# Optimization experiments

Measured on AMD Instinct MI355X. Metric: run time of the kernel, lower is better.

Reference implementation:

```python
import jax, jax.numpy as jnp
import numpy as np

N = 20000      # nodes
E = 640000     # edges
HID = 128      # hidden_dim
HEADS = 8
HD = HID // HEADS  # head_dim = 16


def setup_inputs() -> dict:
    key = jax.random.key(0)
    ks = jax.random.split(key, 32)
    s = 1.0 / np.sqrt(HID)
    d = {}
    d["h"] = jax.random.normal(ks[0], (N, HID), jnp.float32)
    d["x"] = jax.random.normal(ks[1], (N, 3), jnp.float32)
    d["src"] = jax.random.randint(ks[2], (E,), 0, N)
    d["dst"] = jax.random.randint(ks[3], (E,), 0, N)
    d["distances"] = jax.random.uniform(ks[4], (E,), jnp.float32)
    d["bpp_edge_bias"] = jax.random.uniform(ks[5], (E,), jnp.float32)
    d["msa_edge_bias"] = jax.random.uniform(ks[6], (E,), jnp.float32)
    d["chem_edge_bias"] = jax.random.uniform(ks[7], (E,), jnp.float32)
    d["relative_offset"] = jax.random.normal(ks[8], (E,), jnp.float32)
    d["chain_break_mask"] = jax.random.uniform(ks[9], (E,), jnp.float32)
    # attention projections (nn.Linear(hidden, hidden): y = x @ W + b)
    for i, nm in enumerate(["Wq", "Wk", "Wv", "Wo"]):
        d[nm] = jax.random.normal(ks[10 + i], (HID, HID), jnp.float32) * s
    for nm in ["bq", "bk", "bv", "bo"]:
        d[nm] = jnp.zeros((HID,), jnp.float32)
    # six Linear(1, heads) edge-bias heads -> weight vector [HEADS] + bias [HEADS]
    for i, nm in enumerate(["dist", "bpp", "msa", "chem", "rel", "chain"]):
        d["w_" + nm] = jax.random.normal(ks[14 + i], (HEADS,), jnp.float32) * 0.1
        d["b_" + nm] = jnp.zeros((HEADS,), jnp.float32)
    # coord_gate: Linear(HID,HID) -> SiLU -> Linear(HID,1) -> Tanh
    d["Wg1"] = jax.random.normal(ks[20], (HID, HID), jnp.float32) * s
    d["bg1"] = jnp.zeros((HID,), jnp.float32)
    d["wg2"] = jax.random.normal(ks[21], (HID, 1), jnp.float32) * s
    d["bg2"] = jnp.zeros((1,), jnp.float32)
    return d


def _edge_bias(feat, w, b):
    # Linear(1, heads) applied to per-edge scalar: [E] -> [E, HEADS]
    return feat[:, None] * w[None, :] + b[None, :]


def reference(h, x, src, dst, distances, bpp_edge_bias, msa_edge_bias,
              chem_edge_bias, relative_offset, chain_break_mask,
              Wq, bq, Wk, bk, Wv, bv, Wo, bo,
              w_dist, b_dist, w_bpp, b_bpp, w_msa, b_msa,
              w_chem, b_chem, w_rel, b_rel, w_chain, b_chain,
              Wg1, bg1, wg2, bg2):
    n = h.shape[0]
    q = (h @ Wq + bq).reshape(n, HEADS, HD)
    k = (h @ Wk + bk).reshape(n, HEADS, HD)
    v = (h @ Wv + bv).reshape(n, HEADS, HD)
    q_src = q[src]   # [E, H, D]
    k_dst = k[dst]
    v_dst = v[dst]
    logits = jnp.einsum('ehd,ehd->eh', q_src, k_dst) / np.sqrt(float(HD))
    logits = (logits
              - _edge_bias(distances * distances, w_dist, b_dist)
              + _edge_bias(bpp_edge_bias, w_bpp, b_bpp)
              + _edge_bias(msa_edge_bias, w_msa, b_msa)
              + _edge_bias(chem_edge_bias, w_chem, b_chem)
              + _edge_bias(relative_offset, w_rel, b_rel)
              + _edge_bias(chain_break_mask, w_chain, b_chain))
    # segment softmax over edges grouped by src node, per head
    m = jax.ops.segment_max(logits, src, num_segments=n)        # [N, H]
    ex = jnp.exp(logits - m[src])                               # [E, H]
    denom = jax.ops.segment_sum(ex, src, num_segments=n)        # [N, H]
    weights = ex / jnp.maximum(denom[src], 1e-9)                # [E, H]
    # weighted scatter-aggregate of values to src nodes
    h_update = jax.ops.segment_sum(v_dst * weights[:, :, None], src,
                                   num_segments=n).reshape(n, HID)
    h_out = h + h_update @ Wo + bo
    # coordinate update
    weights_mean = weights.mean(axis=1)                         # [E]
    disp = jax.ops.segment_sum((x[dst] - x[src]) * weights_mean[:, None],
                               src, num_segments=n)             # [N, 3]
    gate = jnp.tanh(jax.nn.silu(h_out @ Wg1 + bg1) @ wg2 + bg2)  # [N, 1]
    x_out = x + gate * disp
    return h_out, x_out
```

## Files before the change

kernel.cpp:

```cpp
#include <hip/hip_runtime.h>
#include <hip/hip_bf16.h>

#define N_NODES 20000
#define N_EDGES 640000
#define HID 128
#define HEADS 8
#define HD 16
#define NB_SCAN ((N_NODES + 255) / 256)
#define CH 160
#define QKV_BLOCKS 625
#define PREP_BLOCKS 5

typedef __attribute__((ext_vector_type(8))) short bf16x8;
typedef __attribute__((ext_vector_type(4))) float f32x4;

__device__ __forceinline__ float bflo(unsigned u) {
    union { unsigned i; float f; } x; x.i = u << 16; return x.f;
}
__device__ __forceinline__ float bfhi(unsigned u) {
    union { unsigned i; float f; } x; x.i = u & 0xffff0000u; return x.f;
}
__device__ __forceinline__ float bfu(ushort u) {
    union { unsigned i; float f; } x; x.i = ((unsigned)u) << 16; return x.f;
}
__device__ __forceinline__ ushort f2bu(float f) {
    __hip_bfloat16 b = __float2bfloat16(f);
    union { __hip_bfloat16 b; ushort u; } c; c.b = b; return c.u;
}

__global__ __launch_bounds__(256) void hist_prep_kernel(const int* __restrict__ src,
        int* __restrict__ cnt, int* __restrict__ rank,
        const float* __restrict__ Wq, const float* __restrict__ Wk,
        const float* __restrict__ Wv, const float* __restrict__ Wo,
        const float* __restrict__ Wg1, ushort* __restrict__ Wt) {
    if (blockIdx.x < PREP_BLOCKS) {
        const float* srcs[5] = {Wq, Wk, Wv, Wo, Wg1};
        const float* W = srcs[blockIdx.x];
        ushort* out = Wt + (size_t)blockIdx.x * 16384;
        for (int i = threadIdx.x; i < 16384; i += 256) {
            int k = i >> 7, n = i & 127;
            out[n * 128 + k] = f2bu(W[i]);
        }
    } else {
        const int e = (blockIdx.x - PREP_BLOCKS) * 256 + threadIdx.x;
        rank[e] = atomicAdd(&cnt[src[e]], 1);
    }
}

__global__ __launch_bounds__(256) void scan1_kernel(const int* __restrict__ cnt,
        int* __restrict__ startp, int* __restrict__ blockSums, int n) {
    __shared__ int sd[256];
    const int tid = threadIdx.x;
    const int i = blockIdx.x * 256 + tid;
    int xv = (i < n) ? cnt[i] : 0;
    sd[tid] = xv;
    __syncthreads();
#pragma unroll
    for (int off = 1; off < 256; off <<= 1) {
        int tv = (tid >= off) ? sd[tid - off] : 0;
        __syncthreads();
        sd[tid] += tv;
        __syncthreads();
    }
    if (i < n) startp[i] = sd[tid] - xv;
    if (tid == 255) blockSums[blockIdx.x] = sd[255];
}

__global__ __launch_bounds__(128) void scan2_kernel(int* __restrict__ blockSums, int nb) {
    __shared__ int sd[128];
    const int tid = threadIdx.x;
    int xv = (tid < nb) ? blockSums[tid] : 0;
    sd[tid] = xv;
    __syncthreads();
#pragma unroll
    for (int off = 1; off < 128; off <<= 1) {
        int tv = (tid >= off) ? sd[tid - off] : 0;
        __syncthreads();
        sd[tid] += tv;
        __syncthreads();
    }
    if (tid < nb) blockSums[tid] = sd[tid] - xv;
    if (tid == 127) blockSums[nb] = sd[127];
}

__global__ __launch_bounds__(256) void scatter_qkv_kernel(
        const float* __restrict__ h, const ushort* __restrict__ Wt,
        const float* __restrict__ bq, const float* __restrict__ bk,
        const float* __restrict__ bv,
        ushort* __restrict__ qb, ushort* __restrict__ kb, ushort* __restrict__ vb,
        const int* __restrict__ src, const int* __restrict__ dst,
        const float* __restrict__ dist, const float* __restrict__ bpp,
        const float* __restrict__ msa, const float* __restrict__ chem,
        const float* __restrict__ rel, const float* __restrict__ chain,
        const float* __restrict__ w_dist, const float* __restrict__ b_dist,
        const float* __restrict__ w_bpp, const float* __restrict__ b_bpp,
        const float* __restrict__ w_msa, const float* __restrict__ b_msa,
        const float* __restrict__ w_chem, const float* __restrict__ b_chem,
        const float* __restrict__ w_rel, const float* __restrict__ b_rel,
        const float* __restrict__ w_chain, const float* __restrict__ b_chain,
        const int* __restrict__ startp, const int* __restrict__ blockSums,
        const int* __restrict__ rank, const float* __restrict__ x,
        uint4* __restrict__ recs) {
    __shared__ __align__(16) ushort hs[32 * 136];
    const int t = threadIdx.x;
    if (blockIdx.x < QKV_BLOCKS) {
        const int row0 = blockIdx.x * 32;
        for (int i = t; i < 4096; i += 256)
            hs[(i >> 7) * 136 + (i & 127)] = f2bu(h[(size_t)row0 * 128 + i]);
        __syncthreads();
        const int w = t >> 6, lane = t & 63;
        const int rt = w >> 1, half = w & 1;
        const int lrow = lane & 15, lkb = (lane >> 4) * 8;
        bf16x8 a[4];
#pragma unroll
        for (int ks = 0; ks < 4; ++ks)
            a[ks] = *reinterpret_cast<const bf16x8*>(&hs[(rt * 16 + lrow) * 136 + ks * 32 + lkb]);
        const int rbase = row0 + rt * 16 + (lane >> 4) * 4;
#define DO_MAT(MI, BIAS, OUT) \
        for (int ctp = 0; ctp < 4; ++ctp) { \
            const int col = (ctp * 2 + half) * 16 + lrow; \
            f32x4 acc = {0.f, 0.f, 0.f, 0.f}; \
            _Pragma("unroll") \
            for (int ks = 0; ks < 4; ++ks) { \
                bf16x8 b = *reinterpret_cast<const bf16x8*>( \
                    &Wt[MI * 16384 + col * 128 + ks * 32 + lkb]); \
                acc = __builtin_amdgcn_mfma_f32_16x16x32_bf16(a[ks], b, acc, 0, 0, 0); \
            } \
            const float bias = BIAS[col]; \
            _Pragma("unroll") \
            for (int r = 0; r < 4; ++r) \
                OUT[(size_t)(rbase + r) * 128 + col] = f2bu(acc[r] + bias); \
        }
        DO_MAT(0, bq, qb)
        DO_MAT(1, bk, kb)
        DO_MAT(2, bv, vb)
#undef DO_MAT
    } else {
        const int e = (blockIdx.x - QKV_BLOCKS) * 256 + t;
        const int s = src[e];
        const int pos = startp[s] + blockSums[s >> 8] + rank[e];
        const int dn = dst[e];
        const float d2 = dist[e] * dist[e];
        const float f_bpp = bpp[e], f_msa = msa[e], f_chem = chem[e];
        const float f_rel = rel[e], f_chain = chain[e];
        ushort o16[8];
#pragma unroll
        for (int hq = 0; hq < 8; ++hq) {
            float b = -(d2 * w_dist[hq] + b_dist[hq])
                    + (f_bpp * w_bpp[hq] + b_bpp[hq])
                    + (f_msa * w_msa[hq] + b_msa[hq])
                    + (f_chem * w_chem[hq] + b_chem[hq])
                    + (f_rel * w_rel[hq] + b_rel[hq])
                    + (f_chain * w_chain[hq] + b_chain[hq]);
            o16[hq] = f2bu(b);
        }
        uint4 rec0;
        rec0.x = (unsigned)o16[0] | ((unsigned)o16[1] << 16);
        rec0.y = (unsigned)o16[2] | ((unsigned)o16[3] << 16);
        rec0.z = (unsigned)o16[4] | ((unsigned)o16[5] << 16);
        rec0.w = (unsigned)o16[6] | ((unsigned)o16[7] << 16);
        const float* xp = &x[(size_t)dn * 3];
        uint4 rec1;
        rec1.x = (unsigned)dn;
        rec1.y = __float_as_uint(xp[0]);
        rec1.z = __float_as_uint(xp[1]);
        rec1.w = __float_as_uint(xp[2]);
        recs[(size_t)pos * 2]     = rec0;
        recs[(size_t)pos * 2 + 1] = rec1;
    }
}

__global__ __launch_bounds__(256) void node_kernel(const ushort* __restrict__ qb,
        const ushort* __restrict__ kb, const ushort* __restrict__ vb,
        const uint4* __restrict__ recs, const float* __restrict__ x,
        const int* __restrict__ startp, const int* __restrict__ blockSums,
        ushort* __restrict__ hub, float* __restrict__ disp) {
    __shared__ float qLds[4 * 128];
    __shared__ float xsLds[12];
    __shared__ int   sLds[5];
    __shared__ int   dnLds[CH];
    __shared__ float xLds[CH * 3];
    __shared__ __align__(16) ushort biasLds[CH * 8];
    __shared__ float peLds[CH * 8];
    __shared__ float redN[4][32][9];

    const int t = threadIdx.x;
    const int n0 = blockIdx.x * 4;

    for (int i = t; i < 4 * 128; i += 256) qLds[i] = bfu(qb[(size_t)n0 * 128 + i]);
    if (t < 12) xsLds[t] = x[(size_t)n0 * 3 + t];
    if (t < 5) {
        int idx = n0 + t;
        sLds[t] = (idx < N_NODES) ? (startp[idx] + blockSums[idx >> 8]) : N_EDGES;
    }
    __syncthreads();

    const int S0 = sLds[0], S4 = sLds[4];
    const int s1r = sLds[1], s2r = sLds[2], s3r = sLds[3];

    const int eg = t >> 5;
    const int dq = t & 31;
    const int hh = dq >> 2;
    const int jj = dq & 3;
    const int j3 = (jj < 3) ? jj : 0;

    float acc0[4] = {0,0,0,0}, acc1[4] = {0,0,0,0};
    float acc2[4] = {0,0,0,0}, acc3[4] = {0,0,0,0};
    float den0 = 0, den1 = 0, den2 = 0, den3 = 0;
    float adx0 = 0, adx1 = 0, adx2 = 0, adx3 = 0;

    for (int base = S0; base < S4; base += CH) {
        const int en = min(CH, S4 - base);
        __syncthreads();
        if (t < en) {
            const uint4 r0 = recs[(size_t)(base + t) * 2];
            const uint4 r1 = recs[(size_t)(base + t) * 2 + 1];
            *reinterpret_cast<uint4*>(&biasLds[t * 8]) = r0;
            dnLds[t] = (int)r1.x;
            xLds[t * 3 + 0] = __uint_as_float(r1.y);
            xLds[t * 3 + 1] = __uint_as_float(r1.z);
            xLds[t * 3 + 2] = __uint_as_float(r1.w);
        }
        __syncthreads();
        const int np = en * 8;
        for (int p = t; p < np; p += 256) {
            const int e = p >> 3, ha = p & 7;
            const int ge = base + e;
            const int m = (ge >= s1r) + (ge >= s2r) + (ge >= s3r);
            const ushort* krow = kb + (size_t)dnLds[e] * 128 + ha * 16;
            const uint4 ka = *reinterpret_cast<const uint4*>(krow);
            const uint4 kb4 = *reinterpret_cast<const uint4*>(krow + 8);
            const float* qrow = &qLds[m * 128 + ha * 16];
            const unsigned* kau = reinterpret_cast<const unsigned*>(&ka);
            const unsigned* kbu = reinterpret_cast<const unsigned*>(&kb4);
            float s = 0.f;
#pragma unroll
            for (int i = 0; i < 4; ++i) {
                s += bflo(kau[i]) * qrow[2 * i]     + bfhi(kau[i]) * qrow[2 * i + 1];
                s += bflo(kbu[i]) * qrow[8 + 2 * i] + bfhi(kbu[i]) * qrow[8 + 2 * i + 1];
            }
            peLds[p] = __expf(fmaf(s, 0.25f, bfu(biasLds[p])));
        }
        __syncthreads();
#define NODE_C(M, ACC, DEN, ADX) { \
            const int lo = max(sLds[M] - base, 0); \
            const int hi = min(sLds[M + 1] - base, en); \
            const float xsv = xsLds[M * 3 + j3]; \
            for (int e = lo + eg; e < hi; e += 8) { \
                const float pe = peLds[e * 8 + hh]; \
                const ushort4 vv = *reinterpret_cast<const ushort4*>( \
                    vb + (size_t)dnLds[e] * 128 + dq * 4); \
                ACC[0] = fmaf(pe, bfu(vv.x), ACC[0]); \
                ACC[1] = fmaf(pe, bfu(vv.y), ACC[1]); \
                ACC[2] = fmaf(pe, bfu(vv.z), ACC[2]); \
                ACC[3] = fmaf(pe, bfu(vv.w), ACC[3]); \
                DEN += pe; \
                ADX = fmaf(pe, xLds[e * 3 + j3] - xsv, ADX); \
            } }
        NODE_C(0, acc0, den0, adx0)
        NODE_C(1, acc1, den1, adx1)
        NODE_C(2, acc2, den2, adx2)
        NODE_C(3, acc3, den3, adx3)
#undef NODE_C
    }

    const int wv = t >> 6, lane = t & 63;
#define RED_M(M, ACC, DEN, ADX) { \
        float r0 = ACC[0], r1 = ACC[1], r2 = ACC[2], r3 = ACC[3]; \
        float rd = DEN, rx = (jj < 3) ? ADX : 0.f; \
        r0 += __shfl_xor(r0, 32); r1 += __shfl_xor(r1, 32); \
        r2 += __shfl_xor(r2, 32); r3 += __shfl_xor(r3, 32); \
        rd += __shfl_xor(rd, 32); rx += __shfl_xor(rx, 32); \
        if (lane < 32) { \
            redN[wv][lane][0] = r0; redN[wv][lane][1] = r1; \
            redN[wv][lane][2] = r2; redN[wv][lane][3] = r3; \
            redN[wv][lane][4] = rd; redN[wv][lane][5] = rx; \
        } \
        __syncthreads(); \
        if (t < 128) { \
            const int dqr = t >> 2, vi = t & 3; \
            float s = redN[0][dqr][vi] + redN[1][dqr][vi] \
                    + redN[2][dqr][vi] + redN[3][dqr][vi]; \
            float d = redN[0][dqr][4] + redN[1][dqr][4] \
                    + redN[2][dqr][4] + redN[3][dqr][4]; \
            hub[(size_t)(n0 + M) * 128 + t] = f2bu(s / fmaxf(d, 1e-9f)); \
        } \
        if (t < 32) { \
            float v = redN[0][t][5] + redN[1][t][5] + redN[2][t][5] + redN[3][t][5]; \
            float d = redN[0][t][4] + redN[1][t][4] + redN[2][t][4] + redN[3][t][4]; \
            float s = v / fmaxf(d, 1e-9f); \
            s += __shfl_xor(s, 4); s += __shfl_xor(s, 8); s += __shfl_xor(s, 16); \
            if (t < 3) disp[(size_t)(n0 + M) * 3 + t] = s * 0.125f; \
        } \
        __syncthreads(); }
    RED_M(0, acc0, den0, adx0)
    RED_M(1, acc1, den1, adx1)
    RED_M(2, acc2, den2, adx2)
    RED_M(3, acc3, den3, adx3)
#undef RED_M
}

__global__ __launch_bounds__(256) void out_kernel(const float* __restrict__ h,
        const float* __restrict__ x, const ushort* __restrict__ hub,
        const ushort* __restrict__ Wt,
        const float* __restrict__ bo, const float* __restrict__ bg1,
        const float* __restrict__ wg2, const float* __restrict__ bg2,
        const float* __restrict__ disp,
        float* __restrict__ hout, float* __restrict__ xout) {
    __shared__ __align__(16) ushort hus[32 * 136];
    __shared__ __align__(16) ushort hob[32 * 136];
    __shared__ float g1s[32 * 132];
    const int t = threadIdx.x;
    const int row0 = blockIdx.x * 32;
    for (int i = t; i < 4096; i += 256)
        hus[(i >> 7) * 136 + (i & 127)] = hub[(size_t)row0 * 128 + i];
    __syncthreads();
    const int w = t >> 6, lane = t & 63;
    const int rt = w >> 1, half = w & 1;
    const int lrow = lane & 15, lkb = (lane >> 4) * 8;
    const int rloc = rt * 16 + (lane >> 4) * 4;
    bf16x8 a[4];
#pragma unroll
    for (int ks = 0; ks < 4; ++ks)
        a[ks] = *reinterpret_cast<const bf16x8*>(&hus[(rt * 16 + lrow) * 136 + ks * 32 + lkb]);
    for (int ctp = 0; ctp < 4; ++ctp) {
        const int col = (ctp * 2 + half) * 16 + lrow;
        f32x4 acc = {0.f, 0.f, 0.f, 0.f};
#pragma unroll
        for (int ks = 0; ks < 4; ++ks) {
            bf16x8 b = *reinterpret_cast<const bf16x8*>(&Wt[3 * 16384 + col * 128 + ks * 32 + lkb]);
            acc = __builtin_amdgcn_mfma_f32_16x16x32_bf16(a[ks], b, acc, 0, 0, 0);
        }
        const float bias = bo[col];
#pragma unroll
        for (int r = 0; r < 4; ++r) {
            const int row = rloc + r;
            float hv = h[(size_t)(row0 + row) * 128 + col] + acc[r] + bias;
            hout[(size_t)(row0 + row) * 128 + col] = hv;
            hob[row * 136 + col] = f2bu(hv);
        }
    }
    __syncthreads();
#pragma unroll
    for (int ks = 0; ks < 4; ++ks)
        a[ks] = *reinterpret_cast<const bf16x8*>(&hob[(rt * 16 + lrow) * 136 + ks * 32 + lkb]);
    for (int ctp = 0; ctp < 4; ++ctp) {
        const int col = (ctp * 2 + half) * 16 + lrow;
        f32x4 acc = {0.f, 0.f, 0.f, 0.f};
#pragma unroll
        for (int ks = 0; ks < 4; ++ks) {
            bf16x8 b = *reinterpret_cast<const bf16x8*>(&Wt[4 * 16384 + col * 128 + ks * 32 + lkb]);
            acc = __builtin_amdgcn_mfma_f32_16x16x32_bf16(a[ks], b, acc, 0, 0, 0);
        }
        const float bias = bg1[col];
#pragma unroll
        for (int r = 0; r < 4; ++r) {
            float av = acc[r] + bias;
            g1s[(rloc + r) * 132 + col] = av / (1.f + __expf(-av));
        }
    }
    __syncthreads();
    {
        const int r = t >> 3, j = t & 7;
        float partial = 0.f;
        for (int cc = j; cc < 128; cc += 8) partial += g1s[r * 132 + cc] * wg2[cc];
        partial += __shfl_xor(partial, 1);
        partial += __shfl_xor(partial, 2);
        partial += __shfl_xor(partial, 4);
        const float gate = tanhf(partial + bg2[0]);
        if (j < 3) {
            const int row = row0 + r;
            xout[(size_t)row * 3 + j] = x[(size_t)row * 3 + j] + gate * disp[(size_t)row * 3 + j];
        }
    }
}


extern "C" void kernel_launch(void* const* d_in, const int* in_sizes, int n_in,
                              void* d_out, int out_size, void* d_ws, size_t ws_size,
                              hipStream_t stream) {
    const float* h     = (const float*)d_in[0];
    const float* x     = (const float*)d_in[1];
    const int*   src   = (const int*)d_in[2];
    const int*   dst   = (const int*)d_in[3];
    const float* dist  = (const float*)d_in[4];
    const float* bpp   = (const float*)d_in[5];
    const float* msa   = (const float*)d_in[6];
    const float* chem  = (const float*)d_in[7];
    const float* rel   = (const float*)d_in[8];
    const float* chain = (const float*)d_in[9];
    const float* Wq = (const float*)d_in[10];
    const float* Wk = (const float*)d_in[11];
    const float* Wv = (const float*)d_in[12];
    const float* Wo = (const float*)d_in[13];
    const float* bq = (const float*)d_in[14];
    const float* bk = (const float*)d_in[15];
    const float* bv = (const float*)d_in[16];
    const float* bo = (const float*)d_in[17];
    const float* w_dist = (const float*)d_in[18];  const float* b_dist = (const float*)d_in[19];
    const float* w_bpp  = (const float*)d_in[20];  const float* b_bpp  = (const float*)d_in[21];
    const float* w_msa  = (const float*)d_in[22];  const float* b_msa  = (const float*)d_in[23];
    const float* w_chem = (const float*)d_in[24];  const float* b_chem = (const float*)d_in[25];
    const float* w_rel  = (const float*)d_in[26];  const float* b_rel  = (const float*)d_in[27];
    const float* w_chain= (const float*)d_in[28];  const float* b_chain= (const float*)d_in[29];
    const float* Wg1 = (const float*)d_in[30];
    const float* bg1 = (const float*)d_in[31];
    const float* wg2 = (const float*)d_in[32];
    const float* bg2 = (const float*)d_in[33];

    char* wp = (char*)d_ws;
    const size_t NH2 = (size_t)N_NODES * HID * sizeof(ushort);
    ushort* hub   = (ushort*)wp;               wp += NH2;
    ushort* qb    = (ushort*)wp;               wp += NH2;
    ushort* kb    = (ushort*)wp;               wp += NH2;
    ushort* vb    = (ushort*)wp;               wp += NH2;
    uint4*  recs  = (uint4*)wp;                wp += (size_t)N_EDGES * 32;
    float*  disp  = (float*)wp;                wp += (size_t)N_NODES * 3 * sizeof(float);
    int* rank     = (int*)wp;                  wp += (size_t)N_EDGES * sizeof(int);
    int* startp   = (int*)wp;                  wp += (size_t)N_NODES * sizeof(int);
    int* cnt      = (int*)wp;                  wp += (size_t)N_NODES * sizeof(int);
    int* blockSums= (int*)wp;                  wp += (size_t)(NB_SCAN + 1) * sizeof(int);
    ushort* Wt    = (ushort*)wp;               wp += (size_t)5 * 16384 * sizeof(ushort);

    float* hout = (float*)d_out;
    float* xout = hout + (size_t)N_NODES * HID;

    hipMemsetAsync(cnt, 0, (size_t)N_NODES * sizeof(int), stream);
    hipLaunchKernelGGL(hist_prep_kernel, dim3(N_EDGES / 256 + PREP_BLOCKS), dim3(256), 0, stream,
                       src, cnt, rank, Wq, Wk, Wv, Wo, Wg1, Wt);
    hipLaunchKernelGGL(scan1_kernel, dim3(NB_SCAN), dim3(256), 0, stream,
                       cnt, startp, blockSums, N_NODES);
    hipLaunchKernelGGL(scan2_kernel, dim3(1), dim3(128), 0, stream, blockSums, NB_SCAN);
    hipLaunchKernelGGL(scatter_qkv_kernel, dim3(QKV_BLOCKS + N_EDGES / 256), dim3(256), 0, stream,
                       h, Wt, bq, bk, bv, qb, kb, vb,
                       src, dst, dist, bpp, msa, chem, rel, chain,
                       w_dist, b_dist, w_bpp, b_bpp, w_msa, b_msa,
                       w_chem, b_chem, w_rel, b_rel, w_chain, b_chain,
                       startp, blockSums, rank, x, recs);
    hipLaunchKernelGGL(node_kernel, dim3(N_NODES / 4), dim3(256), 0, stream,
                       qb, kb, vb, recs, x, startp, blockSums, hub, disp);
    hipLaunchKernelGGL(out_kernel, dim3(N_NODES / 32), dim3(256), 0, stream,
                       h, x, hub, Wt, bo, bg1, wg2, bg2, disp, hout, xout);
}
```

Baseline: 163.8 us.

## Stage QKV and out-projection tiles in LDS for coalesced vector I/O, unroll edge loops

The QKV projection now writes each bf16 output tile to shared memory and then copies it to global memory with coalesced 16-byte stores, in place of scattered 2-byte stores. The node kernel loads q with vector loads, splits the dot product across four independent accumulators, and unrolls the attention and aggregation edge loops by two to expose more memory-level parallelism. The output kernel stages h into LDS with float4 loads and writes hout with float4 stores, rebuilding the bf16 gate input from the fp32 tile. This adds extra barriers and LDS traffic, and the larger LDS footprint in the output kernel may lower occupancy.

```diff
diff --git a/kernel.cpp b/kernel.cpp
--- a/kernel.cpp
+++ b/kernel.cpp
@@ -115,8 +115,10 @@
 #pragma unroll
         for (int ks = 0; ks < 4; ++ks)
             a[ks] = *reinterpret_cast<const bf16x8*>(&hs[(rt * 16 + lrow) * 136 + ks * 32 + lkb]);
-        const int rbase = row0 + rt * 16 + (lane >> 4) * 4;
+        __syncthreads();
+        const int rloc0 = rt * 16 + (lane >> 4) * 4;
 #define DO_MAT(MI, BIAS, OUT) \
+        { \
         for (int ctp = 0; ctp < 4; ++ctp) { \
             const int col = (ctp * 2 + half) * 16 + lrow; \
             f32x4 acc = {0.f, 0.f, 0.f, 0.f}; \
@@ -129,7 +131,16 @@
             const float bias = BIAS[col]; \
             _Pragma("unroll") \
             for (int r = 0; r < 4; ++r) \
-                OUT[(size_t)(rbase + r) * 128 + col] = f2bu(acc[r] + bias); \
+                hs[(rloc0 + r) * 128 + col] = f2bu(acc[r] + bias); \
+        } \
+        __syncthreads(); \
+        { \
+            uint4* outp = reinterpret_cast<uint4*>(OUT + (size_t)row0 * 128); \
+            const uint4* inp = reinterpret_cast<const uint4*>(hs); \
+            outp[t] = inp[t]; \
+            outp[t + 256] = inp[t + 256]; \
+        } \
+        __syncthreads(); \
         }
         DO_MAT(0, bq, qb)
         DO_MAT(1, bk, kb)
@@ -187,7 +198,14 @@
     const int t = threadIdx.x;
     const int n0 = blockIdx.x * 4;
 
-    for (int i = t; i < 4 * 128; i += 256) qLds[i] = bfu(qb[(size_t)n0 * 128 + i]);
+    if (t < 64) {
+        uint4 qv = reinterpret_cast<const uint4*>(qb + (size_t)n0 * 128)[t];
+        const unsigned* qu = reinterpret_cast<const unsigned*>(&qv);
+        float4 f0 = make_float4(bflo(qu[0]), bfhi(qu[0]), bflo(qu[1]), bfhi(qu[1]));
+        float4 f1 = make_float4(bflo(qu[2]), bfhi(qu[2]), bflo(qu[3]), bfhi(qu[3]));
+        *reinterpret_cast<float4*>(&qLds[t * 8])     = f0;
+        *reinterpret_cast<float4*>(&qLds[t * 8 + 4]) = f1;
+    }
     if (t < 12) xsLds[t] = x[(size_t)n0 * 3 + t];
     if (t < 5) {
         int idx = n0 + t;
@@ -223,45 +241,61 @@
         }
         __syncthreads();
         const int np = en * 8;
-        for (int p = t; p < np; p += 256) {
-            const int e = p >> 3, ha = p & 7;
-            const int ge = base + e;
-            const int m = (ge >= s1r) + (ge >= s2r) + (ge >= s3r);
-            const ushort* krow = kb + (size_t)dnLds[e] * 128 + ha * 16;
-            const uint4 ka = *reinterpret_cast<const uint4*>(krow);
-            const uint4 kb4 = *reinterpret_cast<const uint4*>(krow + 8);
-            const float* qrow = &qLds[m * 128 + ha * 16];
-            const unsigned* kau = reinterpret_cast<const unsigned*>(&ka);
-            const unsigned* kbu = reinterpret_cast<const unsigned*>(&kb4);
-            float s = 0.f;
-#pragma unroll
-            for (int i = 0; i < 4; ++i) {
-                s += bflo(kau[i]) * qrow[2 * i]     + bfhi(kau[i]) * qrow[2 * i + 1];
-                s += bflo(kbu[i]) * qrow[8 + 2 * i] + bfhi(kbu[i]) * qrow[8 + 2 * i + 1];
-            }
-            peLds[p] = __expf(fmaf(s, 0.25f, bfu(biasLds[p])));
-        }
-        __syncthreads();
+#define PA_BODY(P) { \
+            const int e = (P) >> 3, ha = (P) & 7; \
+            const int ge = base + e; \
+            const int m = (ge >= s1r) + (ge >= s2r) + (ge >= s3r); \
+            const ushort* krow = kb + (size_t)dnLds[e] * 128 + ha * 16; \
+            const uint4 ka = *reinterpret_cast<const uint4*>(krow); \
+            const uint4 kb4 = *reinterpret_cast<const uint4*>(krow + 8); \
+            const float* qrow = &qLds[m * 128 + ha * 16]; \
+            const unsigned* kau = reinterpret_cast<const unsigned*>(&ka); \
+            const unsigned* kbu = reinterpret_cast<const unsigned*>(&kb4); \
+            float s0 = 0.f, s1 = 0.f, s2 = 0.f, s3 = 0.f; \
+            _Pragma("unroll") \
+            for (int i = 0; i < 4; ++i) { \
+                s0 = fmaf(bflo(kau[i]), qrow[2 * i],     s0); \
+                s1 = fmaf(bfhi(kau[i]), qrow[2 * i + 1], s1); \
+                s2 = fmaf(bflo(kbu[i]), qrow[8 + 2 * i],     s2); \
+                s3 = fmaf(bfhi(kbu[i]), qrow[8 + 2 * i + 1], s3); \
+            } \
+            peLds[P] = __expf(fmaf((s0 + s1) + (s2 + s3), 0.25f, bfu(biasLds[P]))); \
+        }
+        {
+            int p = t;
+            for (; p + 256 < np; p += 512) { PA_BODY(p) PA_BODY(p + 256) }
+            if (p < np) PA_BODY(p)
+        }
+#undef PA_BODY
+        __syncthreads();
+#define PC_BODY(E, ACC, DEN, ADX, XSV) { \
+            const float pe = peLds[(E) * 8 + hh]; \
+            const ushort4 vv = *reinterpret_cast<const ushort4*>( \
+                vb + (size_t)dnLds[E] * 128 + dq * 4); \
+            ACC[0] = fmaf(pe, bfu(vv.x), ACC[0]); \
+            ACC[1] = fmaf(pe, bfu(vv.y), ACC[1]); \
+            ACC[2] = fmaf(pe, bfu(vv.z), ACC[2]); \
+            ACC[3] = fmaf(pe, bfu(vv.w), ACC[3]); \
+            DEN += pe; \
+            ADX = fmaf(pe, xLds[(E) * 3 + j3] - XSV, ADX); \
+        }
 #define NODE_C(M, ACC, DEN, ADX) { \
             const int lo = max(sLds[M] - base, 0); \
             const int hi = min(sLds[M + 1] - base, en); \
             const float xsv = xsLds[M * 3 + j3]; \
-            for (int e = lo + eg; e < hi; e += 8) { \
-                const float pe = peLds[e * 8 + hh]; \
-                const ushort4 vv = *reinterpret_cast<const ushort4*>( \
-                    vb + (size_t)dnLds[e] * 128 + dq * 4); \
-                ACC[0] = fmaf(pe, bfu(vv.x), ACC[0]); \
-                ACC[1] = fmaf(pe, bfu(vv.y), ACC[1]); \
-                ACC[2] = fmaf(pe, bfu(vv.z), ACC[2]); \
-                ACC[3] = fmaf(pe, bfu(vv.w), ACC[3]); \
-                DEN += pe; \
-                ADX = fmaf(pe, xLds[e * 3 + j3] - xsv, ADX); \
-            } }
+            int e = lo + eg; \
+            for (; e + 8 < hi; e += 16) { \
+                PC_BODY(e, ACC, DEN, ADX, xsv) \
+                PC_BODY(e + 8, ACC, DEN, ADX, xsv) \
+            } \
+            if (e < hi) PC_BODY(e, ACC, DEN, ADX, xsv) \
+        }
         NODE_C(0, acc0, den0, adx0)
         NODE_C(1, acc1, den1, adx1)
         NODE_C(2, acc2, den2, adx2)
         NODE_C(3, acc3, den3, adx3)
 #undef NODE_C
+#undef PC_BODY
     }
 
     const int wv = t >> 6, lane = t & 63;
@@ -308,12 +342,20 @@
         const float* __restrict__ disp,
         float* __restrict__ hout, float* __restrict__ xout) {
     __shared__ __align__(16) ushort hus[32 * 136];
-    __shared__ __align__(16) ushort hob[32 * 136];
+    __shared__ __align__(16) float hof[32 * 132];
     __shared__ float g1s[32 * 132];
     const int t = threadIdx.x;
     const int row0 = blockIdx.x * 32;
-    for (int i = t; i < 4096; i += 256)
-        hus[(i >> 7) * 136 + (i & 127)] = hub[(size_t)row0 * 128 + i];
+    for (int i8 = t; i8 < 512; i8 += 256) {
+        const int row = i8 >> 4, c8 = (i8 & 15) * 8;
+        *reinterpret_cast<uint4*>(&hus[row * 136 + c8]) =
+            reinterpret_cast<const uint4*>(hub + (size_t)row0 * 128)[i8];
+    }
+    for (int i4 = t; i4 < 1024; i4 += 256) {
+        const int row = i4 >> 5, c4 = (i4 & 31) * 4;
+        *reinterpret_cast<float4*>(&hof[row * 132 + c4]) =
+            reinterpret_cast<const float4*>(h + (size_t)row0 * 128)[i4];
+    }
     __syncthreads();
     const int w = t >> 6, lane = t & 63;
     const int rt = w >> 1, half = w & 1;
@@ -333,24 +375,35 @@
         }
         const float bias = bo[col];
 #pragma unroll
-        for (int r = 0; r < 4; ++r) {
-            const int row = rloc + r;
-            float hv = h[(size_t)(row0 + row) * 128 + col] + acc[r] + bias;
-            hout[(size_t)(row0 + row) * 128 + col] = hv;
-            hob[row * 136 + col] = f2bu(hv);
-        }
-    }
-    __syncthreads();
-#pragma unroll
-    for (int ks = 0; ks < 4; ++ks)
-        a[ks] = *reinterpret_cast<const bf16x8*>(&hob[(rt * 16 + lrow) * 136 + ks * 32 + lkb]);
+        for (int r = 0; r < 4; ++r)
+            hof[(rloc + r) * 132 + col] += acc[r] + bias;
+    }
+    __syncthreads();
+    for (int i4 = t; i4 < 1024; i4 += 256) {
+        const int row = i4 >> 5, c4 = (i4 & 31) * 4;
+        *reinterpret_cast<float4*>(hout + (size_t)(row0 + row) * 128 + c4) =
+            *reinterpret_cast<const float4*>(&hof[row * 132 + c4]);
+    }
+    bf16x8 a2[4];
+#pragma unroll
+    for (int ks = 0; ks < 4; ++ks) {
+        const float* fp = &hof[(rt * 16 + lrow) * 132 + ks * 32 + lkb];
+        const float4 f0 = *reinterpret_cast<const float4*>(fp);
+        const float4 f1 = *reinterpret_cast<const float4*>(fp + 4);
+        bf16x8 v;
+        v[0] = (short)f2bu(f0.x); v[1] = (short)f2bu(f0.y);
+        v[2] = (short)f2bu(f0.z); v[3] = (short)f2bu(f0.w);
+        v[4] = (short)f2bu(f1.x); v[5] = (short)f2bu(f1.y);
+        v[6] = (short)f2bu(f1.z); v[7] = (short)f2bu(f1.w);
+        a2[ks] = v;
+    }
     for (int ctp = 0; ctp < 4; ++ctp) {
         const int col = (ctp * 2 + half) * 16 + lrow;
         f32x4 acc = {0.f, 0.f, 0.f, 0.f};
 #pragma unroll
         for (int ks = 0; ks < 4; ++ks) {
             bf16x8 b = *reinterpret_cast<const bf16x8*>(&Wt[4 * 16384 + col * 128 + ks * 32 + lkb]);
-            acc = __builtin_amdgcn_mfma_f32_16x16x32_bf16(a[ks], b, acc, 0, 0, 0);
+            acc = __builtin_amdgcn_mfma_f32_16x16x32_bf16(a2[ks], b, acc, 0, 0, 0);
         }
         const float bias = bg1[col];
 #pragma unroll
```

Result: no change. 163.0 us (-0.5%).
